# Kernel optimization log

Measured on AMD Instinct MI355X. Metric: run time of the kernel, lower is better.

Reference implementation:

```python
import jax, jax.numpy as jnp
import numpy as np

WIN = 11      # window_size
SIGMA = 1.5
CH = 1        # channel
LEVELS = 5
C1 = 0.01 ** 2
C2 = 0.03 ** 2
MS_WEIGHTS = np.array([0.0448, 0.2856, 0.3001, 0.2363, 0.1333], dtype=np.float32)


def _gaussian_window(dtype):
    x = jnp.arange(WIN, dtype=jnp.float32) - WIN // 2
    g = jnp.exp(-(x ** 2) / (2.0 * SIGMA ** 2))
    g = g / g.sum()
    w2 = jnp.outer(g, g)  # [K, K]
    # depthwise kernel [C, 1, K, K]
    return jnp.broadcast_to(w2[None, None], (CH, 1, WIN, WIN)).astype(dtype)


def _blur(x, w):
    # depthwise 11x11 Gaussian blur, SAME padding (= pad window_size//2)
    return jax.lax.conv_general_dilated(
        x, w, window_strides=(1, 1), padding='SAME',
        dimension_numbers=('NCHW', 'OIHW', 'NCHW'),
        feature_group_count=CH)


def _ssim_level(img1, img2, w):
    mu1 = _blur(img1, w)
    mu2 = _blur(img2, w)
    mu1_sq = mu1 * mu1
    mu2_sq = mu2 * mu2
    mu1_mu2 = mu1 * mu2
    sigma1_sq = _blur(img1 * img1, w) - mu1_sq
    sigma2_sq = _blur(img2 * img2, w) - mu2_sq
    sigma12 = _blur(img1 * img2, w) - mu1_mu2
    denom_c = sigma1_sq + sigma2_sq + C2
    mcs_map = (2.0 * sigma12 + C2) / denom_c
    ssim_map = ((2.0 * mu1_mu2 + C1) / (mu1_sq + mu2_sq + C1)) * mcs_map
    return ssim_map.mean(), mcs_map.mean()


def _avg_pool2(x):
    B, C, H, W = x.shape
    return x.reshape(B, C, H // 2, 2, W // 2, 2).mean(axis=(3, 5))


def reference(img1, img2):
    w = _gaussian_window(img1.dtype)
    weights = jnp.asarray(MS_WEIGHTS, dtype=img1.dtype)
    mssim, mcs = [], []
    for _ in range(LEVELS):  # small fixed loop over pyramid levels
        s, m = _ssim_level(img1, img2, w)
        mssim.append(s)
        mcs.append(m)
        img1 = _avg_pool2(img1)
        img2 = _avg_pool2(img2)
    mssim = jnp.stack(mssim)
    mcs = jnp.stack(mcs)
    return jnp.prod(mcs[:LEVELS - 1] ** weights[:LEVELS - 1]) * mssim[LEVELS - 1] ** weights[LEVELS - 1]


def setup_inputs() -> dict:
    key = jax.random.key(0)
    k1, k2 = jax.random.split(key)
    img1 = jax.random.uniform(k1, (32, 1, 512, 512), dtype=jnp.float32)
    # correlated second image so ssim/mcs means stay positive (fractional powers)
    img2 = jnp.clip(img1 + 0.1 * jax.random.normal(k2, img1.shape, dtype=jnp.float32), 0.0, 1.0)
    return {"img1": img1, "img2": img2}
```

## Files before the change

### kernel.cpp

```cpp
#include <hip/hip_runtime.h>
#include <math.h>


typedef float v2f __attribute__((ext_vector_type(2)));

#define TILE 32
#define HALO 5
#define SROWS 42
#define SMEM_FLOATS 6728

struct GaussW { float w[11]; };

#define C1_ (0.01f * 0.01f)
#define C2_ (0.03f * 0.03f)

__device__ __forceinline__ void ssim_tile(
        const float* __restrict__ p1, const float* __restrict__ p2,
        int W, int tile_x, int tile_y, const GaussW& gw,
        float2* __restrict__ resslot, float* smem, int tid) {
    v2f* hb01 = (v2f*)smem;
    v2f* hb23 = (v2f*)(smem + 2 * SROWS * TILE);
    float* hb4 = smem + 4 * SROWS * TILE;
    float* red = smem + 5 * SROWS * TILE;

    const bool xfast = (tile_x >= 8) && (tile_x + TILE + 8 <= W);

    for (int it = tid; it < SROWS * 8; it += 256) {
        int r = it >> 3, c4 = it & 7;
        int gy = tile_y + r - HALO;
        int gx0 = tile_x + (c4 << 2) - 8;
        bool rowok = (gy >= 0) && (gy < W);
        const float* row1 = p1 + (size_t)gy * W;
        const float* row2 = p2 + (size_t)gy * W;
        float a1[20], a2[20];
#pragma unroll
        for (int i = 0; i < 20; i++) { a1[i] = 0.f; a2[i] = 0.f; }
        if (xfast) {
            if (rowok) {
#pragma unroll
                for (int q = 0; q < 5; q++) {
                    float4 v1 = *(const float4*)(row1 + gx0 + q * 4);
                    float4 v2v = *(const float4*)(row2 + gx0 + q * 4);
                    a1[q*4+0] = v1.x;  a1[q*4+1] = v1.y;  a1[q*4+2] = v1.z;  a1[q*4+3] = v1.w;
                    a2[q*4+0] = v2v.x; a2[q*4+1] = v2v.y; a2[q*4+2] = v2v.z; a2[q*4+3] = v2v.w;
                }
            }
        } else {
#pragma unroll
            for (int q = 0; q < 5; q++) {
                int g = gx0 + q * 4;
                if (rowok && g >= 0 && g + 4 <= W) {
                    float4 v1 = *(const float4*)(row1 + g);
                    float4 v2v = *(const float4*)(row2 + g);
                    a1[q*4+0] = v1.x;  a1[q*4+1] = v1.y;  a1[q*4+2] = v1.z;  a1[q*4+3] = v1.w;
                    a2[q*4+0] = v2v.x; a2[q*4+1] = v2v.y; a2[q*4+2] = v2v.z; a2[q*4+3] = v2v.w;
                }
            }
        }
        v2f A[20];
#pragma unroll
        for (int i = 0; i < 20; i++) A[i] = (v2f){a1[i], a2[i]};
        v2f P[14];
        float p12[14];
#pragma unroll
        for (int i = 0; i < 14; i++) {
            v2f u = A[i + 3];
            P[i] = u * u;
            p12[i] = u.x * u.y;
        }
        v2f h01[4] = {(v2f)(0.f), (v2f)(0.f), (v2f)(0.f), (v2f)(0.f)};
        v2f h23[4] = {(v2f)(0.f), (v2f)(0.f), (v2f)(0.f), (v2f)(0.f)};
        float h4[4] = {0.f, 0.f, 0.f, 0.f};
#pragma unroll
        for (int k = 0; k < 11; k++) {
            float wk = gw.w[k];
#pragma unroll
            for (int j = 0; j < 4; j++) {
                h01[j] += wk * A[3 + j + k];
                h23[j] += wk * P[j + k];
                h4[j]  += wk * p12[j + k];
            }
        }
        int ob = r * TILE + (c4 << 2);
#pragma unroll
        for (int j = 0; j < 4; j++) { hb01[ob + j] = h01[j]; hb23[ob + j] = h23[j]; }
        *(float4*)&hb4[ob] = make_float4(h4[0], h4[1], h4[2], h4[3]);
    }
    __syncthreads();

    float ssim_v = 0.f, mcs_v = 0.f;
    {
        int tx = tid & 31, y0 = (tid >> 5) * 4;
        v2f m01[4], m23[4];
        float m4[4];
        {
            v2f v[14];
#pragma unroll
            for (int r = 0; r < 14; r++) v[r] = hb01[(y0 + r) * TILE + tx];
#pragma unroll
            for (int j = 0; j < 4; j++) {
                v2f s = (v2f)(0.f);
#pragma unroll
                for (int k = 0; k < 11; k++) s += gw.w[k] * v[j + k];
                m01[j] = s;
            }
        }
        {
            v2f v[14];
#pragma unroll
            for (int r = 0; r < 14; r++) v[r] = hb23[(y0 + r) * TILE + tx];
#pragma unroll
            for (int j = 0; j < 4; j++) {
                v2f s = (v2f)(0.f);
#pragma unroll
                for (int k = 0; k < 11; k++) s += gw.w[k] * v[j + k];
                m23[j] = s;
            }
        }
        {
            float v[14];
#pragma unroll
            for (int r = 0; r < 14; r++) v[r] = hb4[(y0 + r) * TILE + tx];
#pragma unroll
            for (int j = 0; j < 4; j++) {
                float s = 0.f;
#pragma unroll
                for (int k = 0; k < 11; k++) s += gw.w[k] * v[j + k];
                m4[j] = s;
            }
        }
#pragma unroll
        for (int j = 0; j < 4; j++) {
            float mu1 = m01[j].x, mu2 = m01[j].y;
            float mu1sq = mu1 * mu1, mu2sq = mu2 * mu2, mu12 = mu1 * mu2;
            float sg11 = m23[j].x - mu1sq;
            float sg22 = m23[j].y - mu2sq;
            float sg12 = m4[j] - mu12;
            float mcs  = (2.f * sg12 + C2_) / (sg11 + sg22 + C2_);
            float ssim = ((2.f * mu12 + C1_) / (mu1sq + mu2sq + C1_)) * mcs;
            ssim_v += ssim;
            mcs_v  += mcs;
        }
    }

#pragma unroll
    for (int off = 32; off > 0; off >>= 1) {
        ssim_v += __shfl_down(ssim_v, off);
        mcs_v  += __shfl_down(mcs_v, off);
    }
    int wave = tid >> 6, lane = tid & 63;
    if (lane == 0) { red[wave] = ssim_v; red[4 + wave] = mcs_v; }
    __syncthreads();
    if (tid == 0) {
        float S = red[0] + red[1] + red[2] + red[3];
        float M = red[4] + red[5] + red[6] + red[7];
        *resslot = make_float2(S, M);
    }
}

__device__ __forceinline__ void pyramid_region(
        const float* __restrict__ in1, const float* __restrict__ in2,
        int n, int reg,
        float* __restrict__ l1a, float* __restrict__ l1b,
        float* __restrict__ l2a, float* __restrict__ l2b,
        float* __restrict__ l3a, float* __restrict__ l3b,
        float* __restrict__ l4a, float* __restrict__ l4b,
        float* smem, int tid) {
    float* b1 = smem;
    float* b2 = smem + 1024;
    float* c1 = smem + 2048;
    float* c2 = smem + 2304;
    float* d1 = smem + 2560;
    float* d2 = smem + 2624;
    const int rx = reg & 7, ry = reg >> 3;
    const float* p1 = in1 + (size_t)n * 512 * 512;
    const float* p2 = in2 + (size_t)n * 512 * 512;

    for (int i = tid; i < 32 * 16; i += 256) {
        int oy = i >> 4, oxp = i & 15;
        int gy = ry * 64 + 2 * oy, gx = rx * 64 + 4 * oxp;
        float4 r10 = *(const float4*)(p1 + (size_t)gy * 512 + gx);
        float4 r11 = *(const float4*)(p1 + (size_t)(gy + 1) * 512 + gx);
        float4 r20 = *(const float4*)(p2 + (size_t)gy * 512 + gx);
        float4 r21 = *(const float4*)(p2 + (size_t)(gy + 1) * 512 + gx);
        float2 o1 = make_float2(0.25f * (r10.x + r10.y + r11.x + r11.y),
                                0.25f * (r10.z + r10.w + r11.z + r11.w));
        float2 o2 = make_float2(0.25f * (r20.x + r20.y + r21.x + r21.y),
                                0.25f * (r20.z + r20.w + r21.z + r21.w));
        *(float2*)&b1[oy * 32 + 2 * oxp] = o1;
        *(float2*)&b2[oy * 32 + 2 * oxp] = o2;
        size_t o = (size_t)n * 256 * 256 + (size_t)(ry * 32 + oy) * 256 + rx * 32 + 2 * oxp;
        *(float2*)&l1a[o] = o1;
        *(float2*)&l1b[o] = o2;
    }
    __syncthreads();
    if (tid < 16 * 8) {
        int oy = tid >> 3, oxp = tid & 7;
        float4 r10 = *(const float4*)&b1[(2 * oy) * 32 + 4 * oxp];
        float4 r11 = *(const float4*)&b1[(2 * oy + 1) * 32 + 4 * oxp];
        float4 r20 = *(const float4*)&b2[(2 * oy) * 32 + 4 * oxp];
        float4 r21 = *(const float4*)&b2[(2 * oy + 1) * 32 + 4 * oxp];
        float2 o1 = make_float2(0.25f * (r10.x + r10.y + r11.x + r11.y),
                                0.25f * (r10.z + r10.w + r11.z + r11.w));
        float2 o2 = make_float2(0.25f * (r20.x + r20.y + r21.x + r21.y),
                                0.25f * (r20.z + r20.w + r21.z + r21.w));
        *(float2*)&c1[oy * 16 + 2 * oxp] = o1;
        *(float2*)&c2[oy * 16 + 2 * oxp] = o2;
        size_t o = (size_t)n * 128 * 128 + (size_t)(ry * 16 + oy) * 128 + rx * 16 + 2 * oxp;
        *(float2*)&l2a[o] = o1;
        *(float2*)&l2b[o] = o2;
    }
    __syncthreads();
    if (tid < 8 * 4) {
        int oy = tid >> 2, oxp = tid & 3;
        float4 r10 = *(const float4*)&c1[(2 * oy) * 16 + 4 * oxp];
        float4 r11 = *(const float4*)&c1[(2 * oy + 1) * 16 + 4 * oxp];
        float4 r20 = *(const float4*)&c2[(2 * oy) * 16 + 4 * oxp];
        float4 r21 = *(const float4*)&c2[(2 * oy + 1) * 16 + 4 * oxp];
        float2 o1 = make_float2(0.25f * (r10.x + r10.y + r11.x + r11.y),
                                0.25f * (r10.z + r10.w + r11.z + r11.w));
        float2 o2 = make_float2(0.25f * (r20.x + r20.y + r21.x + r21.y),
                                0.25f * (r20.z + r20.w + r21.z + r21.w));
        *(float2*)&d1[oy * 8 + 2 * oxp] = o1;
        *(float2*)&d2[oy * 8 + 2 * oxp] = o2;
        size_t o = (size_t)n * 64 * 64 + (size_t)(ry * 8 + oy) * 64 + rx * 8 + 2 * oxp;
        *(float2*)&l3a[o] = o1;
        *(float2*)&l3b[o] = o2;
    }
    __syncthreads();
    if (tid < 4 * 2) {
        int oy = tid >> 1, oxp = tid & 1;
        float4 r10 = *(const float4*)&d1[(2 * oy) * 8 + 4 * oxp];
        float4 r11 = *(const float4*)&d1[(2 * oy + 1) * 8 + 4 * oxp];
        float4 r20 = *(const float4*)&d2[(2 * oy) * 8 + 4 * oxp];
        float4 r21 = *(const float4*)&d2[(2 * oy + 1) * 8 + 4 * oxp];
        float2 o1 = make_float2(0.25f * (r10.x + r10.y + r11.x + r11.y),
                                0.25f * (r10.z + r10.w + r11.z + r11.w));
        float2 o2 = make_float2(0.25f * (r20.x + r20.y + r21.x + r21.y),
                                0.25f * (r20.z + r20.w + r21.z + r21.w));
        size_t o = (size_t)n * 32 * 32 + (size_t)(ry * 4 + oy) * 32 + rx * 4 + 2 * oxp;
        *(float2*)&l4a[o] = o1;
        *(float2*)&l4b[o] = o2;
    }
}

__global__ __launch_bounds__(256, 6) void d1_kernel(
        const float* __restrict__ i0a, const float* __restrict__ i0b,
        float* __restrict__ l1a, float* __restrict__ l1b,
        float* __restrict__ l2a, float* __restrict__ l2b,
        float* __restrict__ l3a, float* __restrict__ l3b,
        float* __restrict__ l4a, float* __restrict__ l4b,
        float2* __restrict__ res0, GaussW gw) {
    __shared__ float smem[SMEM_FLOATS];
    const int tid = threadIdx.x;
    const int t = blockIdx.x;
    const int n = blockIdx.y;
    if (t < 64) {
        pyramid_region(i0a, i0b, n, t, l1a, l1b, l2a, l2b, l3a, l3b, l4a, l4b,
                       smem, tid);
    } else {
        int idx = t - 64;
        const float* p1 = i0a + (size_t)n * 512 * 512;
        const float* p2 = i0b + (size_t)n * 512 * 512;
        ssim_tile(p1, p2, 512, (idx & 15) << 5, (idx >> 4) << 5,
                  gw, &res0[n * 256 + idx], smem, tid);
    }
}

__global__ __launch_bounds__(256, 6) void d2_kernel(
        const float* __restrict__ l1a, const float* __restrict__ l1b,
        const float* __restrict__ l2a, const float* __restrict__ l2b,
        const float* __restrict__ l3a, const float* __restrict__ l3b,
        const float* __restrict__ l4a, const float* __restrict__ l4b,
        float2* __restrict__ res1, float2* __restrict__ res2,
        float2* __restrict__ res3, float2* __restrict__ res4, GaussW gw) {
    __shared__ float smem[SMEM_FLOATS];
    const int tid = threadIdx.x;
    const int t = blockIdx.x;
    const int n = blockIdx.y;
    const float* b1;
    const float* b2;
    int W, tx, ty;
    float2* slot;
    if (t < 64)      { W = 256; b1 = l1a; b2 = l1b; tx = (t & 7) << 5; ty = (t >> 3) << 5; slot = &res1[n * 64 + t]; }
    else if (t < 80) { int i = t - 64; W = 128; b1 = l2a; b2 = l2b; tx = (i & 3) << 5; ty = (i >> 2) << 5; slot = &res2[n * 16 + i]; }
    else if (t < 84) { int i = t - 80; W = 64; b1 = l3a; b2 = l3b; tx = (i & 1) << 5; ty = (i >> 1) << 5; slot = &res3[n * 4 + i]; }
    else             { W = 32; b1 = l4a; b2 = l4b; tx = 0; ty = 0; slot = &res4[n]; }
    ssim_tile(b1 + (size_t)n * W * W, b2 + (size_t)n * W * W, W,
              tx, ty, gw, slot, smem, tid);
}

__global__ void finalize_kernel(const float2* __restrict__ res0,
                                const float2* __restrict__ res1,
                                const float2* __restrict__ res2,
                                const float2* __restrict__ res3,
                                const float2* __restrict__ res4,
                                float* __restrict__ out, int N) {
    __shared__ float2 redf[5][4];
    const int tid = threadIdx.x;
    const float2* rr[5] = {res0, res1, res2, res3, res4};
    const int cnts[5] = {N * 256, N * 64, N * 16, N * 4, N};
#pragma unroll
    for (int l = 0; l < 5; l++) {
        float sx = 0.f, sy = 0.f;
        for (int i = tid; i < cnts[l]; i += 256) {
            float2 v = rr[l][i];
            sx += v.x;
            sy += v.y;
        }
#pragma unroll
        for (int off = 32; off > 0; off >>= 1) {
            sx += __shfl_down(sx, off);
            sy += __shfl_down(sy, off);
        }
        if ((tid & 63) == 0) redf[l][tid >> 6] = make_float2(sx, sy);
    }
    __syncthreads();
    if (tid == 0) {
        const float wts[5] = {0.0448f, 0.2856f, 0.3001f, 0.2363f, 0.1333f};
        float r = 1.f;
#pragma unroll
        for (int l = 0; l < 5; l++) {
            float sx = redf[l][0].x + redf[l][1].x + redf[l][2].x + redf[l][3].x;
            float sy = redf[l][0].y + redf[l][1].y + redf[l][2].y + redf[l][3].y;
            int Hl = 512 >> l;
            float cnt = (float)N * (float)Hl * (float)Hl;
            float ssim_m = sx / cnt;
            float mcs_m  = sy / cnt;
            if (l < 4) r *= powf(mcs_m, wts[l]);
            else       r *= powf(ssim_m, wts[4]);
        }
        out[0] = r;
    }
}

extern "C" void kernel_launch(void* const* d_in, const int* in_sizes, int n_in,
                              void* d_out, int out_size, void* d_ws, size_t ws_size,
                              hipStream_t stream) {
    const float* img1 = (const float*)d_in[0];
    const float* img2 = (const float*)d_in[1];
    float* out = (float*)d_out;
    const int HW0 = 512 * 512;
    const int N = in_sizes[0] / HW0;

    float* base = (float*)d_ws;
    size_t cur = 0;
    float* l1a = base + cur; cur += (size_t)N * 256 * 256;
    float* l1b = base + cur; cur += (size_t)N * 256 * 256;
    float* l2a = base + cur; cur += (size_t)N * 128 * 128;
    float* l2b = base + cur; cur += (size_t)N * 128 * 128;
    float* l3a = base + cur; cur += (size_t)N * 64 * 64;
    float* l3b = base + cur; cur += (size_t)N * 64 * 64;
    float* l4a = base + cur; cur += (size_t)N * 32 * 32;
    float* l4b = base + cur; cur += (size_t)N * 32 * 32;
    float2* res0 = (float2*)(base + cur); cur += (size_t)N * 512;
    float2* res1 = (float2*)(base + cur); cur += (size_t)N * 128;
    float2* res2 = (float2*)(base + cur); cur += (size_t)N * 32;
    float2* res3 = (float2*)(base + cur); cur += (size_t)N * 8;
    float2* res4 = (float2*)(base + cur); cur += (size_t)N * 2;

    GaussW gw;
    {
        double g[11], sum = 0.0;
        for (int i = 0; i < 11; i++) {
            double x = (double)(i - 5);
            g[i] = exp(-(x * x) / (2.0 * 1.5 * 1.5));
            sum += g[i];
        }
        for (int i = 0; i < 11; i++) gw.w[i] = (float)(g[i] / sum);
    }

    d1_kernel<<<dim3(320, N), 256, 0, stream>>>(
        img1, img2, l1a, l1b, l2a, l2b, l3a, l3b, l4a, l4b, res0, gw);
    d2_kernel<<<dim3(85, N), 256, 0, stream>>>(
        l1a, l1b, l2a, l2b, l3a, l3b, l4a, l4b, res1, res2, res3, res4, gw);
    finalize_kernel<<<1, 256, 0, stream>>>(res0, res1, res2, res3, res4, out, N);
}
```

Before: 168.9 us.

## Blur sum/difference images to reduce SSIM from five to four blur channels

Replaces the five blurred quantities (x, y, x², y², xy) with four: s=x+y, d=x-y, s² and d². The SSIM and contrast-structure terms are then recovered algebraically from these. This removes one blur channel of horizontal and vertical work and shrinks shared memory, and launch bounds are raised to allow 7 blocks per CU. It slightly changes floating-point rounding, and the tighter register budget may cause spills.

```diff
diff --git a/kernel.cpp b/kernel.cpp
--- a/kernel.cpp
+++ b/kernel.cpp
@@ -7,7 +7,7 @@
 #define TILE 32
 #define HALO 5
 #define SROWS 42
-#define SMEM_FLOATS 6728
+#define SMEM_FLOATS 5384
 
 struct GaussW { float w[11]; };
 
@@ -18,10 +18,9 @@
         const float* __restrict__ p1, const float* __restrict__ p2,
         int W, int tile_x, int tile_y, const GaussW& gw,
         float2* __restrict__ resslot, float* smem, int tid) {
-    v2f* hb01 = (v2f*)smem;
-    v2f* hb23 = (v2f*)(smem + 2 * SROWS * TILE);
-    float* hb4 = smem + 4 * SROWS * TILE;
-    float* red = smem + 5 * SROWS * TILE;
+    v2f* hbSD = (v2f*)smem;
+    v2f* hbSQ = (v2f*)(smem + 2 * SROWS * TILE);
+    float* red = smem + 4 * SROWS * TILE;
 
     const bool xfast = (tile_x >= 8) && (tile_x + TILE + 8 <= W);
 
@@ -57,87 +56,68 @@
                 }
             }
         }
-        v2f A[20];
-#pragma unroll
-        for (int i = 0; i < 20; i++) A[i] = (v2f){a1[i], a2[i]};
-        v2f P[14];
-        float p12[14];
+        v2f SD[14], SQ[14];
 #pragma unroll
         for (int i = 0; i < 14; i++) {
-            v2f u = A[i + 3];
-            P[i] = u * u;
-            p12[i] = u.x * u.y;
-        }
-        v2f h01[4] = {(v2f)(0.f), (v2f)(0.f), (v2f)(0.f), (v2f)(0.f)};
-        v2f h23[4] = {(v2f)(0.f), (v2f)(0.f), (v2f)(0.f), (v2f)(0.f)};
-        float h4[4] = {0.f, 0.f, 0.f, 0.f};
+            float x = a1[i + 3], y = a2[i + 3];
+            v2f sd = {x + y, x - y};
+            SD[i] = sd;
+            SQ[i] = sd * sd;
+        }
+        v2f hsd[4] = {(v2f)(0.f), (v2f)(0.f), (v2f)(0.f), (v2f)(0.f)};
+        v2f hsq[4] = {(v2f)(0.f), (v2f)(0.f), (v2f)(0.f), (v2f)(0.f)};
 #pragma unroll
         for (int k = 0; k < 11; k++) {
             float wk = gw.w[k];
 #pragma unroll
             for (int j = 0; j < 4; j++) {
-                h01[j] += wk * A[3 + j + k];
-                h23[j] += wk * P[j + k];
-                h4[j]  += wk * p12[j + k];
+                hsd[j] += wk * SD[j + k];
+                hsq[j] += wk * SQ[j + k];
             }
         }
         int ob = r * TILE + (c4 << 2);
 #pragma unroll
-        for (int j = 0; j < 4; j++) { hb01[ob + j] = h01[j]; hb23[ob + j] = h23[j]; }
-        *(float4*)&hb4[ob] = make_float4(h4[0], h4[1], h4[2], h4[3]);
+        for (int j = 0; j < 4; j++) { hbSD[ob + j] = hsd[j]; hbSQ[ob + j] = hsq[j]; }
     }
     __syncthreads();
 
     float ssim_v = 0.f, mcs_v = 0.f;
     {
         int tx = tid & 31, y0 = (tid >> 5) * 4;
-        v2f m01[4], m23[4];
-        float m4[4];
+        v2f msd[4], msq[4];
         {
             v2f v[14];
 #pragma unroll
-            for (int r = 0; r < 14; r++) v[r] = hb01[(y0 + r) * TILE + tx];
+            for (int r = 0; r < 14; r++) v[r] = hbSD[(y0 + r) * TILE + tx];
 #pragma unroll
             for (int j = 0; j < 4; j++) {
                 v2f s = (v2f)(0.f);
 #pragma unroll
                 for (int k = 0; k < 11; k++) s += gw.w[k] * v[j + k];
-                m01[j] = s;
+                msd[j] = s;
             }
         }
         {
             v2f v[14];
 #pragma unroll
-            for (int r = 0; r < 14; r++) v[r] = hb23[(y0 + r) * TILE + tx];
+            for (int r = 0; r < 14; r++) v[r] = hbSQ[(y0 + r) * TILE + tx];
 #pragma unroll
             for (int j = 0; j < 4; j++) {
                 v2f s = (v2f)(0.f);
 #pragma unroll
                 for (int k = 0; k < 11; k++) s += gw.w[k] * v[j + k];
-                m23[j] = s;
-            }
-        }
-        {
-            float v[14];
-#pragma unroll
-            for (int r = 0; r < 14; r++) v[r] = hb4[(y0 + r) * TILE + tx];
-#pragma unroll
-            for (int j = 0; j < 4; j++) {
-                float s = 0.f;
-#pragma unroll
-                for (int k = 0; k < 11; k++) s += gw.w[k] * v[j + k];
-                m4[j] = s;
+                msq[j] = s;
             }
         }
 #pragma unroll
         for (int j = 0; j < 4; j++) {
-            float mu1 = m01[j].x, mu2 = m01[j].y;
-            float mu1sq = mu1 * mu1, mu2sq = mu2 * mu2, mu12 = mu1 * mu2;
-            float sg11 = m23[j].x - mu1sq;
-            float sg22 = m23[j].y - mu2sq;
-            float sg12 = m4[j] - mu12;
-            float mcs  = (2.f * sg12 + C2_) / (sg11 + sg22 + C2_);
-            float ssim = ((2.f * mu12 + C1_) / (mu1sq + mu2sq + C1_)) * mcs;
+            float bs = msd[j].x, bd = msd[j].y;
+            float bs2 = msq[j].x, bd2 = msq[j].y;
+            float qp = bs * bs, qm = bd * bd;
+            float u = bs2 - qp;
+            float v = bd2 - qm;
+            float mcs  = (0.5f * (u - v) + C2_) / (0.5f * (u + v) + C2_);
+            float ssim = ((0.5f * (qp - qm) + C1_) / (0.5f * (qp + qm) + C1_)) * mcs;
             ssim_v += ssim;
             mcs_v  += mcs;
         }
@@ -244,7 +224,7 @@
     }
 }
 
-__global__ __launch_bounds__(256, 6) void d1_kernel(
+__global__ __launch_bounds__(256, 7) void d1_kernel(
         const float* __restrict__ i0a, const float* __restrict__ i0b,
         float* __restrict__ l1a, float* __restrict__ l1b,
         float* __restrict__ l2a, float* __restrict__ l2b,
@@ -267,7 +247,7 @@
     }
 }
 
-__global__ __launch_bounds__(256, 6) void d2_kernel(
+__global__ __launch_bounds__(256, 7) void d2_kernel(
         const float* __restrict__ l1a, const float* __restrict__ l1b,
         const float* __restrict__ l2a, const float* __restrict__ l2b,
         const float* __restrict__ l3a, const float* __restrict__ l3b,
```

Result: faster. 156.0 us (-7.6%).
